# Performance work log

Measured on AMD Instinct MI355X. Metric: run time of the kernel, lower is better.

The kernel has to match this reference:

```python
import jax, jax.numpy as jnp
import numpy as np

N = 100000   # num nodes
E = 640000   # num edges
IN, H, OUT = 6, 128, 1
BN_EPS = 1e-5


def setup_inputs() -> dict:
    key = jax.random.key(0)
    ks = jax.random.split(key, 12)
    x = jax.random.normal(ks[0], (N, IN), dtype=jnp.float32)
    edge_index = jax.random.randint(ks[1], (2, E), 0, N, dtype=jnp.int64)
    def lin(k, fin, fout):
        s = 1.0 / np.sqrt(fin)
        return jax.random.uniform(k, (fin, fout), jnp.float32, -s, s)
    return {
        "x": x,
        "edge_index": edge_index,
        "W1": lin(ks[2], IN, H),  "b1": jnp.zeros((H,), jnp.float32),
        "W2": lin(ks[3], H, H),   "b2": jnp.zeros((H,), jnp.float32),
        "W3": lin(ks[4], H, OUT), "b3": jnp.zeros((OUT,), jnp.float32),
        "g1": jnp.ones((H,), jnp.float32),  "be1": jnp.zeros((H,), jnp.float32),
        "g2": jnp.ones((H,), jnp.float32),  "be2": jnp.zeros((H,), jnp.float32),
    }


def _gcn_norm(edge_index):
    # add self-loops, then symmetric normalization D^-1/2 (A+I) D^-1/2
    loop = jnp.arange(N, dtype=edge_index.dtype)
    src = jnp.concatenate([edge_index[0], loop])
    dst = jnp.concatenate([edge_index[1], loop])
    deg = jax.ops.segment_sum(jnp.ones_like(dst, dtype=jnp.float32), dst, num_segments=N)
    dis = jnp.where(deg > 0, jax.lax.rsqrt(deg), 0.0)
    norm = dis[src] * dis[dst]  # (E+N,)
    return src, dst, norm


def _conv(h, W, b, src, dst, norm):
    m = h @ W                                   # (N, out) linear transform first
    msg = m[src] * norm[:, None]                # gather + edge scaling
    return jax.ops.segment_sum(msg, dst, num_segments=N) + b


def _bn(h, g, be):
    mu = h.mean(axis=0)
    var = h.var(axis=0)  # biased, as torch BN uses for normalization
    return g * (h - mu) * jax.lax.rsqrt(var + BN_EPS) + be


def reference(x, edge_index, W1, b1, W2, b2, W3, b3, g1, be1, g2, be2):
    src, dst, norm = _gcn_norm(edge_index)
    h = jax.nn.relu(_bn(_conv(x, W1, b1, src, dst, norm), g1, be1))
    h = jax.nn.relu(_bn(_conv(h, W2, b2, src, dst, norm), g2, be2))
    out = _conv(h, W3, b3, src, dst, norm)
    return jax.nn.sigmoid(out)  # (N, 1) risk scores
```

## Files before the change

kernel.cpp:

```cpp
#include <hip/hip_runtime.h>
#include <hip/hip_bf16.h>
#include <math.h>

#define HDIM 128
#define BN_EPS 1e-5f
#define CHUNK 512
#define TM 64
#define LDA 132

__device__ __forceinline__ int eget(const void* ei, long long pos, int is64) {
    return is64 ? (int)((const long long*)ei)[pos] : ((const int*)ei)[pos];
}
__device__ __forceinline__ unsigned short f2bf(float f) {
    unsigned int u = __float_as_uint(f);
    u += 0x7fffu + ((u >> 16) & 1u);
    return (unsigned short)(u >> 16);
}
__device__ __forceinline__ unsigned int pack2bf(float lo, float hi) {
    return (unsigned int)f2bf(lo) | ((unsigned int)f2bf(hi) << 16);
}
__device__ __forceinline__ float bflo(unsigned int u) {
    return __uint_as_float(u << 16);
}
__device__ __forceinline__ float bfhi(unsigned int u) {
    return __uint_as_float(u & 0xffff0000u);
}

__device__ __forceinline__ int block_is64(const void* ei) {
    __shared__ int snz;
    if (threadIdx.x == 0) snz = 0;
    __syncthreads();
    if (threadIdx.x < 64 && ((const int*)ei)[2 * threadIdx.x + 1] != 0)
        atomicAdd(&snz, 1);
    __syncthreads();
    return (snz < 8) ? 1 : 0;
}

__global__ void k_count(const void* ei, int* cnt, int E,
                        const float* __restrict__ x, float* __restrict__ xp,
                        long long n8,
                        const float* __restrict__ W2f,
                        unsigned short* __restrict__ w2h) {
    int is64 = block_is64(ei);
    long long e = (long long)blockIdx.x * blockDim.x + threadIdx.x;
    long long stride = (long long)gridDim.x * blockDim.x;
    if (e < E) {
        int d = eget(ei, (long long)E + e, is64);
        atomicAdd(&cnt[d], 1);
    }
    for (long long t = e; t < n8; t += stride) {
        int i = (int)(t >> 3), c = (int)(t & 7);
        xp[t] = (c < 6) ? x[i * 6 + c] : 0.f;
    }
    for (long long t = e; t < HDIM * HDIM; t += stride)
        w2h[t] = f2bf(W2f[t]);
}

__global__ void k_scan1(const int* cnt, int* bsum, float* __restrict__ dis, int N) {
    __shared__ int s[256];
    int t = threadIdx.x;
    int i = blockIdx.x * CHUNK + t;
    int v = 0;
    if (i < N) {
        int c = cnt[i]; v += c;
        dis[i] = rsqrtf((float)(c + 1));
    }
    if (i + 256 < N && t + 256 < CHUNK) {
        int c = cnt[i + 256]; v += c;
        dis[i + 256] = rsqrtf((float)(c + 1));
    }
    s[t] = v; __syncthreads();
    for (int o = 128; o > 0; o >>= 1) {
        if (t < o) s[t] += s[t + o];
        __syncthreads();
    }
    if (t == 0) bsum[blockIdx.x] = s[0];
}

__global__ void k_scan2(int* bsum, int nb) {
    __shared__ int s[512];
    int t = threadIdx.x;
    int carry = 0;
    for (int base = 0; base < nb; base += 512) {
        int i = base + t;
        int v = (i < nb) ? bsum[i] : 0;
        s[t] = v; __syncthreads();
        for (int o = 1; o < 512; o <<= 1) {
            int add = (t >= o) ? s[t - o] : 0;
            __syncthreads();
            s[t] += add;
            __syncthreads();
        }
        if (i < nb) bsum[i] = carry + s[t] - v;
        carry += s[511];
        __syncthreads();
    }
}

__global__ void k_scan3(int* cnt, const int* bsum, int* rowptr, int N) {
    __shared__ int s[CHUNK];
    int t = threadIdx.x;
    int i = blockIdx.x * CHUNK + t;
    int v = (i < N) ? cnt[i] : 0;
    s[t] = v; __syncthreads();
    for (int o = 1; o < CHUNK; o <<= 1) {
        int add = (t >= o) ? s[t - o] : 0;
        __syncthreads();
        s[t] += add;
        __syncthreads();
    }
    if (i < N) { rowptr[i] = bsum[blockIdx.x] + s[t] - v; cnt[i] = 0; }
    if (i == N - 1) rowptr[N] = bsum[blockIdx.x] + s[t];
}

__global__ void k_fillcsr(const void* ei, const float* dis,
                          const int* rowptr, int* fill, int2* emeta, int E) {
    int is64 = block_is64(ei);
    int e = blockIdx.x * blockDim.x + threadIdx.x;
    if (e < E) {
        int s = eget(ei, e, is64);
        int d = eget(ei, (long long)E + e, is64);
        int pos = rowptr[d] + atomicAdd(&fill[d], 1);
        emeta[pos] = make_int2(s, __float_as_int(dis[s] * dis[d]));
    }
}

__global__ void k_gath_x(const float* __restrict__ xp, const int* __restrict__ rowptr,
                         const int2* __restrict__ emeta,
                         const float* __restrict__ dis, float* __restrict__ aggx, int N) {
    int i = blockIdx.x * blockDim.x + threadIdx.x;
    if (i >= N) return;
    float d = dis[i], d2 = d * d;
    float4 A = *(const float4*)&xp[i * 8];
    float2 B = *(const float2*)&xp[i * 8 + 4];
    float a0 = A.x * d2, a1 = A.y * d2, a2 = A.z * d2;
    float a3 = A.w * d2, a4 = B.x * d2, a5 = B.y * d2;
    int p = rowptr[i], pe = rowptr[i + 1];
    for (; p + 4 <= pe; p += 4) {
        int2 e0 = emeta[p], e1 = emeta[p + 1], e2 = emeta[p + 2], e3 = emeta[p + 3];
        float n0 = __int_as_float(e0.y), n1 = __int_as_float(e1.y);
        float n2 = __int_as_float(e2.y), n3 = __int_as_float(e3.y);
        float4 A0 = *(const float4*)&xp[e0.x * 8];
        float2 B0 = *(const float2*)&xp[e0.x * 8 + 4];
        float4 A1 = *(const float4*)&xp[e1.x * 8];
        float2 B1 = *(const float2*)&xp[e1.x * 8 + 4];
        float4 A2 = *(const float4*)&xp[e2.x * 8];
        float2 B2 = *(const float2*)&xp[e2.x * 8 + 4];
        float4 A3 = *(const float4*)&xp[e3.x * 8];
        float2 B3 = *(const float2*)&xp[e3.x * 8 + 4];
        a0 += (A0.x * n0 + A1.x * n1) + (A2.x * n2 + A3.x * n3);
        a1 += (A0.y * n0 + A1.y * n1) + (A2.y * n2 + A3.y * n3);
        a2 += (A0.z * n0 + A1.z * n1) + (A2.z * n2 + A3.z * n3);
        a3 += (A0.w * n0 + A1.w * n1) + (A2.w * n2 + A3.w * n3);
        a4 += (B0.x * n0 + B1.x * n1) + (B2.x * n2 + B3.x * n3);
        a5 += (B0.y * n0 + B1.y * n1) + (B2.y * n2 + B3.y * n3);
    }
    for (; p < pe; ++p) {
        int2 e0 = emeta[p];
        float n0 = __int_as_float(e0.y);
        float4 A0 = *(const float4*)&xp[e0.x * 8];
        float2 B0 = *(const float2*)&xp[e0.x * 8 + 4];
        a0 += A0.x * n0; a1 += A0.y * n0; a2 += A0.z * n0;
        a3 += A0.w * n0; a4 += B0.x * n0; a5 += B0.y * n0;
    }
    aggx[i * 6 + 0] = a0; aggx[i * 6 + 1] = a1; aggx[i * 6 + 2] = a2;
    aggx[i * 6 + 3] = a3; aggx[i * 6 + 4] = a4; aggx[i * 6 + 5] = a5;
}

__global__ void k_gemm6(const float* __restrict__ aggx, const float* __restrict__ W1,
                        const float* __restrict__ b1, unsigned short* __restrict__ out,
                        float* __restrict__ S, int N) {
    __shared__ float w[6 * HDIM];
    __shared__ float bb[HDIM];
    __shared__ float sh1[256], sh2[256];
    for (int t = threadIdx.x; t < 6 * HDIM; t += blockDim.x) w[t] = W1[t];
    if (threadIdx.x < HDIM) bb[threadIdx.x] = b1[threadIdx.x];
    __syncthreads();
    int j = threadIdx.x & (HDIM - 1);
    int sub = threadIdx.x >> 7;
    float s1 = 0.f, s2 = 0.f;
    for (long long i = blockIdx.x * 2 + sub; i < N; i += (long long)gridDim.x * 2) {
        const float* r = &aggx[i * 6];
        float acc = bb[j];
        acc += r[0] * w[0 * HDIM + j];
        acc += r[1] * w[1 * HDIM + j];
        acc += r[2] * w[2 * HDIM + j];
        acc += r[3] * w[3 * HDIM + j];
        acc += r[4] * w[4 * HDIM + j];
        acc += r[5] * w[5 * HDIM + j];
        out[i * HDIM + j] = f2bf(acc);
        s1 += acc; s2 += acc * acc;
    }
    sh1[threadIdx.x] = s1; sh2[threadIdx.x] = s2;
    __syncthreads();
    if (threadIdx.x < HDIM) {
        atomicAdd(&S[j], sh1[j] + sh1[j + HDIM]);
        atomicAdd(&S[HDIM + j], sh2[j] + sh2[j + HDIM]);
    }
}

__global__ __launch_bounds__(512, 6)
void k_agg_gemm(const unsigned short* __restrict__ m1,
                const float* __restrict__ S1, const float* __restrict__ g1,
                const float* __restrict__ be1, float invN,
                const int* __restrict__ rowptr, const int2* __restrict__ emeta,
                const float* __restrict__ dis,
                const unsigned short* __restrict__ W, const float* __restrict__ b,
                unsigned short* __restrict__ out, float* __restrict__ S,
                int* __restrict__ ticket, int ntiles, int N) {
    __shared__ float At[TM * LDA];
    __shared__ float Pp[256];
    __shared__ int s_tile;
    const int tid = threadIdx.x;

    if (tid < HDIM) {
        float mu = S1[tid] * invN;
        float var = S1[HDIM + tid] * invN - mu * mu;
        float al = g1[tid] * rsqrtf(var + BN_EPS);
        Pp[tid] = al;
        Pp[HDIM + tid] = be1[tid] - mu * al;
    }
    __syncthreads();

    const int gl = tid & 31;
    const int gq = tid >> 5;
    const int c4 = gl * 4;
    const float4 pa = *(const float4*)&Pp[c4];
    const float4 pb = *(const float4*)&Pp[HDIM + c4];

    const int cg = tid & 31;
    const int rg = tid >> 5;
    const int c0 = cg * 4;
    const int r0 = rg * 4;
    const float4 bv = *(const float4*)&b[c0];

    for (;;) {
        if (tid == 0) s_tile = atomicAdd(ticket, 1);
        __syncthreads();
        const int tile = s_tile;
        if (tile >= ntiles) return;
        const long long i0 = (long long)tile * TM;

        for (int nn = gq; nn < TM; nn += 16) {
            long long i = i0 + nn;
            float a0 = 0.f, a1 = 0.f, a2 = 0.f, a3 = 0.f;
            if (i < N) {
                float d = dis[i], d2 = d * d;
                uint2 us = *(const uint2*)&m1[i * HDIM + c4];
                a0 = fmaxf(fmaf(pa.x, bflo(us.x), pb.x), 0.f) * d2;
                a1 = fmaxf(fmaf(pa.y, bfhi(us.x), pb.y), 0.f) * d2;
                a2 = fmaxf(fmaf(pa.z, bflo(us.y), pb.z), 0.f) * d2;
                a3 = fmaxf(fmaf(pa.w, bfhi(us.y), pb.w), 0.f) * d2;
                int p = rowptr[i], pe = rowptr[i + 1];
                for (; p + 4 <= pe; p += 4) {
                    int2 eA = emeta[p],     eB = emeta[p + 1];
                    int2 eC = emeta[p + 2], eD = emeta[p + 3];
                    float nA = __int_as_float(eA.y), nB = __int_as_float(eB.y);
                    float nC = __int_as_float(eC.y), nD = __int_as_float(eD.y);
                    uint2 uA = *(const uint2*)&m1[(long long)eA.x * HDIM + c4];
                    uint2 uB = *(const uint2*)&m1[(long long)eB.x * HDIM + c4];
                    uint2 uC = *(const uint2*)&m1[(long long)eC.x * HDIM + c4];
                    uint2 uD = *(const uint2*)&m1[(long long)eD.x * HDIM + c4];
                    a0 += (fmaxf(fmaf(pa.x, bflo(uA.x), pb.x), 0.f) * nA
                         + fmaxf(fmaf(pa.x, bflo(uB.x), pb.x), 0.f) * nB)
                        + (fmaxf(fmaf(pa.x, bflo(uC.x), pb.x), 0.f) * nC
                         + fmaxf(fmaf(pa.x, bflo(uD.x), pb.x), 0.f) * nD);
                    a1 += (fmaxf(fmaf(pa.y, bfhi(uA.x), pb.y), 0.f) * nA
                         + fmaxf(fmaf(pa.y, bfhi(uB.x), pb.y), 0.f) * nB)
                        + (fmaxf(fmaf(pa.y, bfhi(uC.x), pb.y), 0.f) * nC
                         + fmaxf(fmaf(pa.y, bfhi(uD.x), pb.y), 0.f) * nD);
                    a2 += (fmaxf(fmaf(pa.z, bflo(uA.y), pb.z), 0.f) * nA
                         + fmaxf(fmaf(pa.z, bflo(uB.y), pb.z), 0.f) * nB)
                        + (fmaxf(fmaf(pa.z, bflo(uC.y), pb.z), 0.f) * nC
                         + fmaxf(fmaf(pa.z, bflo(uD.y), pb.z), 0.f) * nD);
                    a3 += (fmaxf(fmaf(pa.w, bfhi(uA.y), pb.w), 0.f) * nA
                         + fmaxf(fmaf(pa.w, bfhi(uB.y), pb.w), 0.f) * nB)
                        + (fmaxf(fmaf(pa.w, bfhi(uC.y), pb.w), 0.f) * nC
                         + fmaxf(fmaf(pa.w, bfhi(uD.y), pb.w), 0.f) * nD);
                }
                if (p + 2 <= pe) {
                    int2 eA = emeta[p], eB = emeta[p + 1];
                    float nA = __int_as_float(eA.y), nB = __int_as_float(eB.y);
                    uint2 uA = *(const uint2*)&m1[(long long)eA.x * HDIM + c4];
                    uint2 uB = *(const uint2*)&m1[(long long)eB.x * HDIM + c4];
                    a0 += fmaxf(fmaf(pa.x, bflo(uA.x), pb.x), 0.f) * nA
                        + fmaxf(fmaf(pa.x, bflo(uB.x), pb.x), 0.f) * nB;
                    a1 += fmaxf(fmaf(pa.y, bfhi(uA.x), pb.y), 0.f) * nA
                        + fmaxf(fmaf(pa.y, bfhi(uB.x), pb.y), 0.f) * nB;
                    a2 += fmaxf(fmaf(pa.z, bflo(uA.y), pb.z), 0.f) * nA
                        + fmaxf(fmaf(pa.z, bflo(uB.y), pb.z), 0.f) * nB;
                    a3 += fmaxf(fmaf(pa.w, bfhi(uA.y), pb.w), 0.f) * nA
                        + fmaxf(fmaf(pa.w, bfhi(uB.y), pb.w), 0.f) * nB;
                    p += 2;
                }
                if (p < pe) {
                    int2 eA = emeta[p];
                    float nA = __int_as_float(eA.y);
                    uint2 uA = *(const uint2*)&m1[(long long)eA.x * HDIM + c4];
                    a0 += fmaxf(fmaf(pa.x, bflo(uA.x), pb.x), 0.f) * nA;
                    a1 += fmaxf(fmaf(pa.y, bfhi(uA.x), pb.y), 0.f) * nA;
                    a2 += fmaxf(fmaf(pa.z, bflo(uA.y), pb.z), 0.f) * nA;
                    a3 += fmaxf(fmaf(pa.w, bfhi(uA.y), pb.w), 0.f) * nA;
                }
            }
            *(float4*)&At[nn * LDA + c4] = make_float4(a0, a1, a2, a3);
        }
        __syncthreads();

        float acc[4][4];
        #pragma unroll
        for (int rr = 0; rr < 4; ++rr) {
            acc[rr][0] = bv.x; acc[rr][1] = bv.y; acc[rr][2] = bv.z; acc[rr][3] = bv.w;
        }
        for (int k = 0; k < HDIM; k += 4) {
            const uint2 q0 = *(const uint2*)&W[(k + 0) * HDIM + c0];
            const uint2 q1 = *(const uint2*)&W[(k + 1) * HDIM + c0];
            const uint2 q2 = *(const uint2*)&W[(k + 2) * HDIM + c0];
            const uint2 q3 = *(const uint2*)&W[(k + 3) * HDIM + c0];
            const float w00 = bflo(q0.x), w01 = bfhi(q0.x), w02 = bflo(q0.y), w03 = bfhi(q0.y);
            const float w10 = bflo(q1.x), w11 = bfhi(q1.x), w12 = bflo(q1.y), w13 = bfhi(q1.y);
            const float w20 = bflo(q2.x), w21 = bfhi(q2.x), w22 = bflo(q2.y), w23 = bfhi(q2.y);
            const float w30 = bflo(q3.x), w31 = bfhi(q3.x), w32 = bflo(q3.y), w33 = bfhi(q3.y);
            #pragma unroll
            for (int rr = 0; rr < 4; ++rr) {
                const float4 av = *(const float4*)&At[(r0 + rr) * LDA + k];
                acc[rr][0] = fmaf(av.x, w00, acc[rr][0]);
                acc[rr][1] = fmaf(av.x, w01, acc[rr][1]);
                acc[rr][2] = fmaf(av.x, w02, acc[rr][2]);
                acc[rr][3] = fmaf(av.x, w03, acc[rr][3]);
                acc[rr][0] = fmaf(av.y, w10, acc[rr][0]);
                acc[rr][1] = fmaf(av.y, w11, acc[rr][1]);
                acc[rr][2] = fmaf(av.y, w12, acc[rr][2]);
                acc[rr][3] = fmaf(av.y, w13, acc[rr][3]);
                acc[rr][0] = fmaf(av.z, w20, acc[rr][0]);
                acc[rr][1] = fmaf(av.z, w21, acc[rr][1]);
                acc[rr][2] = fmaf(av.z, w22, acc[rr][2]);
                acc[rr][3] = fmaf(av.z, w23, acc[rr][3]);
                acc[rr][0] = fmaf(av.w, w30, acc[rr][0]);
                acc[rr][1] = fmaf(av.w, w31, acc[rr][1]);
                acc[rr][2] = fmaf(av.w, w32, acc[rr][2]);
                acc[rr][3] = fmaf(av.w, w33, acc[rr][3]);
            }
        }

        float cs1[4] = {0.f, 0.f, 0.f, 0.f};
        float cs2[4] = {0.f, 0.f, 0.f, 0.f};
        #pragma unroll
        for (int rr = 0; rr < 4; ++rr) {
            long long i = i0 + r0 + rr;
            if (i < N) {
                uint2 o;
                o.x = pack2bf(acc[rr][0], acc[rr][1]);
                o.y = pack2bf(acc[rr][2], acc[rr][3]);
                *(uint2*)&out[i * HDIM + c0] = o;
                #pragma unroll
                for (int cc = 0; cc < 4; ++cc) {
                    float v = acc[rr][cc];
                    cs1[cc] += v; cs2[cc] += v * v;
                }
            }
        }
        __syncthreads();
        #pragma unroll
        for (int cc = 0; cc < 4; ++cc) {
            At[rg * HDIM + c0 + cc]        = cs1[cc];
            At[2048 + rg * HDIM + c0 + cc] = cs2[cc];
        }
        __syncthreads();
        if (tid < 256) {
            int j = tid & (HDIM - 1);
            int which = tid >> 7;
            const float* bp = &At[which * 2048 + j];
            float s = 0.f;
            #pragma unroll
            for (int g = 0; g < 16; ++g) s += bp[g * HDIM];
            atomicAdd(&S[which * HDIM + j], s);
        }
        __syncthreads();
    }
}

__global__ void k_gemv2(const unsigned short* __restrict__ m2,
                        const float* __restrict__ S2, const float* __restrict__ g2,
                        const float* __restrict__ be2, float invN,
                        const float* __restrict__ W3, float* __restrict__ m3, int N) {
    __shared__ float Pp[256];
    int tid = threadIdx.x;
    if (tid < HDIM) {
        float mu = S2[tid] * invN;
        float var = S2[HDIM + tid] * invN - mu * mu;
        float al = g2[tid] * rsqrtf(var + BN_EPS);
        Pp[tid] = al;
        Pp[HDIM + tid] = be2[tid] - mu * al;
    }
    __syncthreads();
    int l = tid & 31;
    int c4 = l * 4;
    float4 pa = *(const float4*)&Pp[c4];
    float4 pb = *(const float4*)&Pp[HDIM + c4];
    float4 w  = *(const float4*)&W3[c4];
    for (long long row = blockIdx.x * 8 + (tid >> 5); row < N;
         row += (long long)gridDim.x * 8) {
        uint2 v = *(const uint2*)&m2[row * HDIM + c4];
        float s = fmaxf(fmaf(pa.x, bflo(v.x), pb.x), 0.f) * w.x
                + fmaxf(fmaf(pa.y, bfhi(v.x), pb.y), 0.f) * w.y
                + fmaxf(fmaf(pa.z, bflo(v.y), pb.z), 0.f) * w.z
                + fmaxf(fmaf(pa.w, bfhi(v.y), pb.w), 0.f) * w.w;
        for (int o = 16; o > 0; o >>= 1) s += __shfl_down(s, o, 32);
        if (l == 0) m3[row] = s;
    }
}

__global__ void k_gath_o(const float* __restrict__ m3, const int* __restrict__ rowptr,
                         const int2* __restrict__ emeta,
                         const float* __restrict__ dis, const float* __restrict__ b3,
                         float* __restrict__ out, int N) {
    int i = blockIdx.x * blockDim.x + threadIdx.x;
    if (i < N) {
        float d = dis[i];
        float acc = m3[i] * d * d;
        int p = rowptr[i], pe = rowptr[i + 1];
        for (; p + 4 <= pe; p += 4) {
            int2 e0 = emeta[p], e1 = emeta[p + 1], e2 = emeta[p + 2], e3 = emeta[p + 3];
            float v0 = m3[e0.x] * __int_as_float(e0.y);
            float v1 = m3[e1.x] * __int_as_float(e1.y);
            float v2 = m3[e2.x] * __int_as_float(e2.y);
            float v3 = m3[e3.x] * __int_as_float(e3.y);
            acc += (v0 + v1) + (v2 + v3);
        }
        for (; p < pe; ++p) {
            int2 e0 = emeta[p];
            acc += m3[e0.x] * __int_as_float(e0.y);
        }
        acc += b3[0];
        out[i] = 1.f / (1.f + expf(-acc));
    }
}

extern "C" void kernel_launch(void* const* d_in, const int* in_sizes, int n_in,
                              void* d_out, int out_size, void* d_ws, size_t ws_size,
                              hipStream_t stream) {
    const float* x  = (const float*)d_in[0];
    const void*  ei = d_in[1];
    const float* W1 = (const float*)d_in[2];
    const float* b1 = (const float*)d_in[3];
    const float* W2 = (const float*)d_in[4];
    const float* b2 = (const float*)d_in[5];
    const float* W3 = (const float*)d_in[6];
    const float* b3 = (const float*)d_in[7];
    const float* g1 = (const float*)d_in[8];
    const float* be1 = (const float*)d_in[9];
    const float* g2 = (const float*)d_in[10];
    const float* be2 = (const float*)d_in[11];

    const int N = in_sizes[0] / 6;
    const int E = in_sizes[1] / 2;
    const float invN = 1.0f / (float)N;

    float* ws = (float*)d_ws;
    long long off = 0;
    auto pad4 = [](long long v) { return (v + 3) & ~3LL; };
    int*   flag   = (int*)ws;                 off += 16;
    int*   ticket = (int*)ws + 1;
    float* S1     = ws + off;                 off += 256;
    float* S2     = ws + off;                 off += 256;
    float* dis    = ws + off;                 off = pad4(off + N);
    int*   cnt    = (int*)(ws + off);         off = pad4(off + N);
    int*   rowptr = (int*)(ws + off);         off = pad4(off + N + 16);
    int2*  emeta  = (int2*)(ws + off);        off = pad4(off + (long long)2 * E);
    int*   bsum   = (int*)(ws + off);         off += 512;
    unsigned short* w2h = (unsigned short*)(ws + off); off += HDIM * HDIM / 2;
    float* xp     = ws + off;                 off = pad4(off + (long long)8 * N);
    float* aggx   = ws + off;                 off = pad4(off + (long long)6 * N);
    float* m3     = ws + off;                 off = pad4(off + N);
    unsigned short* m1 = (unsigned short*)(ws + off); off = pad4(off + (long long)64 * N);
    unsigned short* m2 = (unsigned short*)(ws + off); off = pad4(off + (long long)64 * N);

    const int T = 256;
    const int bN  = (N + T - 1) / T;
    const int bE  = (E + T - 1) / T;
    const int nchunk = (N + CHUNK - 1) / CHUNK;
    const int ntiles = (N + TM - 1) / TM;

    hipMemsetAsync(ws, 0, 528 * sizeof(float), stream);
    hipMemsetAsync(cnt, 0, (size_t)N * sizeof(int), stream);
    k_count<<<bE, T, 0, stream>>>(ei, cnt, E, x, xp, (long long)8 * N, W2, w2h);
    k_scan1<<<nchunk, 256, 0, stream>>>(cnt, bsum, dis, N);
    k_scan2<<<1, 512, 0, stream>>>(bsum, nchunk);
    k_scan3<<<nchunk, CHUNK, 0, stream>>>(cnt, bsum, rowptr, N);
    k_fillcsr<<<bE, T, 0, stream>>>(ei, dis, rowptr, cnt, emeta, E);

    k_gath_x<<<bN, T, 0, stream>>>(xp, rowptr, emeta, dis, aggx, N);
    k_gemm6<<<512, T, 0, stream>>>(aggx, W1, b1, m1, S1, N);

    k_agg_gemm<<<1024, 512, 0, stream>>>(m1, S1, g1, be1, invN,
                                         rowptr, emeta, dis,
                                         w2h, b2, m2, S2, ticket, ntiles, N);

    k_gemv2<<<1024, T, 0, stream>>>(m2, S2, g2, be2, invN, W3, m3, N);
    k_gath_o<<<bN, T, 0, stream>>>(m3, rowptr, emeta, dis, b3, (float*)d_out, N);
}
```

Before: 265.7 us.

## Use bf16 MFMA for the fused aggregation GEMM with transposed W2

```diff
diff --git a/kernel.cpp b/kernel.cpp
--- a/kernel.cpp
+++ b/kernel.cpp
@@ -6,7 +6,10 @@
 #define BN_EPS 1e-5f
 #define CHUNK 512
 #define TM 64
-#define LDA 132
+#define ALD 136
+
+typedef __attribute__((ext_vector_type(8))) short bf16x8;
+typedef __attribute__((ext_vector_type(4))) float f32x4;
 
 __device__ __forceinline__ int eget(const void* ei, long long pos, int is64) {
     return is64 ? (int)((const long long*)ei)[pos] : ((const int*)ei)[pos];
@@ -40,7 +43,7 @@
                         const float* __restrict__ x, float* __restrict__ xp,
                         long long n8,
                         const float* __restrict__ W2f,
-                        unsigned short* __restrict__ w2h) {
+                        unsigned short* __restrict__ w2t) {
     int is64 = block_is64(ei);
     long long e = (long long)blockIdx.x * blockDim.x + threadIdx.x;
     long long stride = (long long)gridDim.x * blockDim.x;
@@ -52,8 +55,10 @@
         int i = (int)(t >> 3), c = (int)(t & 7);
         xp[t] = (c < 6) ? x[i * 6 + c] : 0.f;
     }
-    for (long long t = e; t < HDIM * HDIM; t += stride)
-        w2h[t] = f2bf(W2f[t]);
+    for (long long t = e; t < HDIM * HDIM; t += stride) {
+        int k = (int)(t >> 7), n = (int)(t & (HDIM - 1));
+        w2t[(long long)n * HDIM + k] = f2bf(W2f[t]);
+    }
 }
 
 __global__ void k_scan1(const int* cnt, int* bsum, float* __restrict__ dis, int N) {
@@ -199,17 +204,19 @@
     }
 }
 
-__global__ __launch_bounds__(512, 6)
+__global__ __launch_bounds__(512, 8)
 void k_agg_gemm(const unsigned short* __restrict__ m1,
                 const float* __restrict__ S1, const float* __restrict__ g1,
                 const float* __restrict__ be1, float invN,
                 const int* __restrict__ rowptr, const int2* __restrict__ emeta,
                 const float* __restrict__ dis,
-                const unsigned short* __restrict__ W, const float* __restrict__ b,
+                const unsigned short* __restrict__ W2T,
+                const float* __restrict__ b,
                 unsigned short* __restrict__ out, float* __restrict__ S,
                 int* __restrict__ ticket, int ntiles, int N) {
-    __shared__ float At[TM * LDA];
+    __shared__ unsigned short At[TM * ALD];
     __shared__ float Pp[256];
+    __shared__ float csA[HDIM], csB[HDIM];
     __shared__ int s_tile;
     const int tid = threadIdx.x;
 
@@ -228,13 +235,19 @@
     const float4 pa = *(const float4*)&Pp[c4];
     const float4 pb = *(const float4*)&Pp[HDIM + c4];
 
-    const int cg = tid & 31;
-    const int rg = tid >> 5;
-    const int c0 = cg * 4;
-    const int r0 = rg * 4;
-    const float4 bv = *(const float4*)&b[c0];
+    const int w   = tid >> 6;
+    const int lane = tid & 63;
+    const int l15 = lane & 15;
+    const int l4  = lane >> 4;
+    const int mi  = (w & 3) * 16;
+    const int nb  = (w >> 2) * 64;
+    const float bj0 = b[nb +  0 + l15];
+    const float bj1 = b[nb + 16 + l15];
+    const float bj2 = b[nb + 32 + l15];
+    const float bj3 = b[nb + 48 + l15];
 
     for (;;) {
+        if (tid < HDIM) { csA[tid] = 0.f; csB[tid] = 0.f; }
         if (tid == 0) s_tile = atomicAdd(ticket, 1);
         __syncthreads();
         const int tile = s_tile;
@@ -303,78 +316,54 @@
                     a3 += fmaxf(fmaf(pa.w, bfhi(uA.y), pb.w), 0.f) * nA;
                 }
             }
-            *(float4*)&At[nn * LDA + c4] = make_float4(a0, a1, a2, a3);
-        }
-        __syncthreads();
-
-        float acc[4][4];
+            uint2 o;
+            o.x = pack2bf(a0, a1);
+            o.y = pack2bf(a2, a3);
+            *(uint2*)&At[nn * ALD + c4] = o;
+        }
+        __syncthreads();
+
+        f32x4 acc0 = {bj0, bj0, bj0, bj0};
+        f32x4 acc1 = {bj1, bj1, bj1, bj1};
+        f32x4 acc2 = {bj2, bj2, bj2, bj2};
+        f32x4 acc3 = {bj3, bj3, bj3, bj3};
         #pragma unroll
-        for (int rr = 0; rr < 4; ++rr) {
-            acc[rr][0] = bv.x; acc[rr][1] = bv.y; acc[rr][2] = bv.z; acc[rr][3] = bv.w;
-        }
-        for (int k = 0; k < HDIM; k += 4) {
-            const uint2 q0 = *(const uint2*)&W[(k + 0) * HDIM + c0];
-            const uint2 q1 = *(const uint2*)&W[(k + 1) * HDIM + c0];
-            const uint2 q2 = *(const uint2*)&W[(k + 2) * HDIM + c0];
-            const uint2 q3 = *(const uint2*)&W[(k + 3) * HDIM + c0];
-            const float w00 = bflo(q0.x), w01 = bfhi(q0.x), w02 = bflo(q0.y), w03 = bfhi(q0.y);
-            const float w10 = bflo(q1.x), w11 = bfhi(q1.x), w12 = bflo(q1.y), w13 = bfhi(q1.y);
-            const float w20 = bflo(q2.x), w21 = bfhi(q2.x), w22 = bflo(q2.y), w23 = bfhi(q2.y);
-            const float w30 = bflo(q3.x), w31 = bfhi(q3.x), w32 = bflo(q3.y), w33 = bfhi(q3.y);
-            #pragma unroll
-            for (int rr = 0; rr < 4; ++rr) {
-                const float4 av = *(const float4*)&At[(r0 + rr) * LDA + k];
-                acc[rr][0] = fmaf(av.x, w00, acc[rr][0]);
-                acc[rr][1] = fmaf(av.x, w01, acc[rr][1]);
-                acc[rr][2] = fmaf(av.x, w02, acc[rr][2]);
-                acc[rr][3] = fmaf(av.x, w03, acc[rr][3]);
-                acc[rr][0] = fmaf(av.y, w10, acc[rr][0]);
-                acc[rr][1] = fmaf(av.y, w11, acc[rr][1]);
-                acc[rr][2] = fmaf(av.y, w12, acc[rr][2]);
-                acc[rr][3] = fmaf(av.y, w13, acc[rr][3]);
-                acc[rr][0] = fmaf(av.z, w20, acc[rr][0]);
-                acc[rr][1] = fmaf(av.z, w21, acc[rr][1]);
-                acc[rr][2] = fmaf(av.z, w22, acc[rr][2]);
-                acc[rr][3] = fmaf(av.z, w23, acc[rr][3]);
-                acc[rr][0] = fmaf(av.w, w30, acc[rr][0]);
-                acc[rr][1] = fmaf(av.w, w31, acc[rr][1]);
-                acc[rr][2] = fmaf(av.w, w32, acc[rr][2]);
-                acc[rr][3] = fmaf(av.w, w33, acc[rr][3]);
-            }
-        }
-
-        float cs1[4] = {0.f, 0.f, 0.f, 0.f};
-        float cs2[4] = {0.f, 0.f, 0.f, 0.f};
-        #pragma unroll
-        for (int rr = 0; rr < 4; ++rr) {
-            long long i = i0 + r0 + rr;
-            if (i < N) {
-                uint2 o;
-                o.x = pack2bf(acc[rr][0], acc[rr][1]);
-                o.y = pack2bf(acc[rr][2], acc[rr][3]);
-                *(uint2*)&out[i * HDIM + c0] = o;
-                #pragma unroll
-                for (int cc = 0; cc < 4; ++cc) {
-                    float v = acc[rr][cc];
-                    cs1[cc] += v; cs2[cc] += v * v;
-                }
-            }
-        }
-        __syncthreads();
-        #pragma unroll
-        for (int cc = 0; cc < 4; ++cc) {
-            At[rg * HDIM + c0 + cc]        = cs1[cc];
-            At[2048 + rg * HDIM + c0 + cc] = cs2[cc];
-        }
+        for (int k0 = 0; k0 < HDIM; k0 += 32) {
+            const int kk = k0 + l4 * 8;
+            bf16x8 af = *(const bf16x8*)&At[(mi + l15) * ALD + kk];
+            bf16x8 b0 = *(const bf16x8*)&W2T[(long long)(nb +  0 + l15) * HDIM + kk];
+            bf16x8 b1 = *(const bf16x8*)&W2T[(long long)(nb + 16 + l15) * HDIM + kk];
+            bf16x8 b2 = *(const bf16x8*)&W2T[(long long)(nb + 32 + l15) * HDIM + kk];
+            bf16x8 b3 = *(const bf16x8*)&W2T[(long long)(nb + 48 + l15) * HDIM + kk];
+            acc0 = __builtin_amdgcn_mfma_f32_16x16x32_bf16(af, b0, acc0, 0, 0, 0);
+            acc1 = __builtin_amdgcn_mfma_f32_16x16x32_bf16(af, b1, acc1, 0, 0, 0);
+            acc2 = __builtin_amdgcn_mfma_f32_16x16x32_bf16(af, b2, acc2, 0, 0, 0);
+            acc3 = __builtin_amdgcn_mfma_f32_16x16x32_bf16(af, b3, acc3, 0, 0, 0);
+        }
+
+        const int rowb = mi + l4 * 4;
+        #define EMIT(ACC, NJ)                                                  \
+        {                                                                      \
+            const int col = nb + (NJ)*16 + l15;                                \
+            float s1 = 0.f, s2 = 0.f;                                          \
+            _Pragma("unroll")                                                  \
+            for (int r = 0; r < 4; ++r) {                                      \
+                long long i = i0 + rowb + r;                                   \
+                if (i < N) {                                                   \
+                    float v = ACC[r];                                          \
+                    out[i * HDIM + col] = f2bf(v);                             \
+                    s1 += v; s2 += v * v;                                      \
+                }                                                              \
+            }                                                                  \
+            atomicAdd(&csA[col], s1);                                          \
+            atomicAdd(&csB[col], s2);                                          \
+        }
+        EMIT(acc0, 0) EMIT(acc1, 1) EMIT(acc2, 2) EMIT(acc3, 3)
+        #undef EMIT
         __syncthreads();
         if (tid < 256) {
-            int j = tid & (HDIM - 1);
-            int which = tid >> 7;
-            const float* bp = &At[which * 2048 + j];
-            float s = 0.f;
-            #pragma unroll
-            for (int g = 0; g < 16; ++g) s += bp[g * HDIM];
-            atomicAdd(&S[which * HDIM + j], s);
+            float v = (tid < HDIM) ? csA[tid] : csB[tid - HDIM];
+            atomicAdd(&S[tid], v);
         }
         __syncthreads();
     }
@@ -460,8 +449,7 @@
     float* ws = (float*)d_ws;
     long long off = 0;
     auto pad4 = [](long long v) { return (v + 3) & ~3LL; };
-    int*   flag   = (int*)ws;                 off += 16;
-    int*   ticket = (int*)ws + 1;
+    int*   ticket = (int*)ws + 1;             off += 16;
     float* S1     = ws + off;                 off += 256;
     float* S2     = ws + off;                 off += 256;
     float* dis    = ws + off;                 off = pad4(off + N);
@@ -469,7 +457,7 @@
     int*   rowptr = (int*)(ws + off);         off = pad4(off + N + 16);
     int2*  emeta  = (int2*)(ws + off);        off = pad4(off + (long long)2 * E);
     int*   bsum   = (int*)(ws + off);         off += 512;
-    unsigned short* w2h = (unsigned short*)(ws + off); off += HDIM * HDIM / 2;
+    unsigned short* w2t = (unsigned short*)(ws + off); off += HDIM * HDIM / 2;
     float* xp     = ws + off;                 off = pad4(off + (long long)8 * N);
     float* aggx   = ws + off;                 off = pad4(off + (long long)6 * N);
     float* m3     = ws + off;                 off = pad4(off + N);
@@ -484,7 +472,7 @@
 
     hipMemsetAsync(ws, 0, 528 * sizeof(float), stream);
     hipMemsetAsync(cnt, 0, (size_t)N * sizeof(int), stream);
-    k_count<<<bE, T, 0, stream>>>(ei, cnt, E, x, xp, (long long)8 * N, W2, w2h);
+    k_count<<<bE, T, 0, stream>>>(ei, cnt, E, x, xp, (long long)8 * N, W2, w2t);
     k_scan1<<<nchunk, 256, 0, stream>>>(cnt, bsum, dis, N);
     k_scan2<<<1, 512, 0, stream>>>(bsum, nchunk);
     k_scan3<<<nchunk, CHUNK, 0, stream>>>(cnt, bsum, rowptr, N);
@@ -495,7 +483,7 @@
 
     k_agg_gemm<<<1024, 512, 0, stream>>>(m1, S1, g1, be1, invN,
                                          rowptr, emeta, dis,
-                                         w2h, b2, m2, S2, ticket, ntiles, N);
+                                         w2t, b2, m2, S2, ticket, ntiles, N);
 
     k_gemv2<<<1024, T, 0, stream>>>(m2, S2, g2, be2, invN, W3, m3, N);
     k_gath_o<<<bN, T, 0, stream>>>(m3, rowptr, emeta, dis, b3, (float*)d_out, N);
```

New measurement: 268.1 us. Within noise of the previous version (+0.9%).
